# Optimization experiments

Measured on AMD Instinct MI355X. Metric: run time of the kernel, lower is better.

## Reference

```python
import jax, jax.numpy as jnp
import numpy as np
from jax import lax

B, C, H, W = 8, 64, 128, 128
KS = 3          # kernel size
K = KS * KS     # kernel field = 9
PAD = 1


def conv2d(x, w, b):
    # x: [B,Cin,H,W], w: [Cout,Cin,kh,kw], 'same' 3x3 conv
    y = lax.conv_general_dilated(x, w, window_strides=(1, 1),
                                 padding=((PAD, PAD), (PAD, PAD)),
                                 dimension_numbers=('NCHW', 'OIHW', 'NCHW'))
    return y + b[None, :, None, None]


def modulated_deform_conv(x, offset, mask, weight, bias):
    # x:[B,C,H,W], offset:[B,2K,H,W] (dy,dx per tap), mask:[B,K,H,W]
    Bs, Cin, Hin, Win = x.shape
    off = offset.reshape(Bs, K, 2, Hin, Win)
    ky, kx = jnp.meshgrid(jnp.arange(KS), jnp.arange(KS), indexing='ij')
    ky = ky.reshape(K).astype(x.dtype)   # kernel tap row offsets 0..2
    kx = kx.reshape(K).astype(x.dtype)
    # sampling positions p = p0 + p_k + offset (stride=1, pad=1)
    py = (jnp.arange(Hin, dtype=x.dtype)[None, None, :, None] - PAD
          + ky[None, :, None, None] + off[:, :, 0])            # [B,K,H,W]
    px = (jnp.arange(Win, dtype=x.dtype)[None, None, None, :] - PAD
          + kx[None, :, None, None] + off[:, :, 1])            # [B,K,H,W]

    y0 = jnp.floor(py); x0 = jnp.floor(px)
    ly = py - y0; lx = px - x0                                  # frac parts
    y0i = y0.astype(jnp.int32); x0i = x0.astype(jnp.int32)

    x_flat = x.reshape(Bs, Cin, Hin * Win)

    def gather(iy, ix):
        valid = ((iy >= 0) & (iy < Hin) & (ix >= 0) & (ix < Win))
        flat = (jnp.clip(iy, 0, Hin - 1) * Win + jnp.clip(ix, 0, Win - 1))
        g = jax.vmap(lambda xb, ib: xb[:, ib])(x_flat, flat.reshape(Bs, -1))
        g = g.reshape(Bs, Cin, K, Hin, Win)
        return g * valid[:, None].astype(x.dtype)

    w00 = ((1 - ly) * (1 - lx))[:, None]  # [B,1,K,H,W]
    w01 = ((1 - ly) * lx)[:, None]
    w10 = (ly * (1 - lx))[:, None]
    w11 = (ly * lx)[:, None]

    val = (w00 * gather(y0i, x0i) + w01 * gather(y0i, x0i + 1)
           + w10 * gather(y0i + 1, x0i) + w11 * gather(y0i + 1, x0i + 1))
    val = val * mask[:, None]                                   # modulation
    out = jnp.einsum('ock,bckhw->bohw', weight.reshape(weight.shape[0], Cin, K), val)
    return out + bias[None, :, None, None]


def setup_inputs() -> dict:
    key = jax.random.key(0)
    ks = jax.random.split(key, 7)
    s = 0.05
    return {
        'x': jax.random.normal(ks[0], (B, C, H, W), jnp.float32),
        'w_om': jax.random.normal(ks[1], (3 * K, C, KS, KS), jnp.float32) * s,
        'b_om': jax.random.normal(ks[2], (3 * K,), jnp.float32) * s,
        'w_dc': jax.random.normal(ks[3], (C, C, KS, KS), jnp.float32) * s,
        'b_dc': jax.random.normal(ks[4], (C,), jnp.float32) * s,
        'w_c': jax.random.normal(ks[5], (C, C, KS, KS), jnp.float32) * s,
        'b_c': jax.random.normal(ks[6], (C,), jnp.float32) * s,
    }


def reference(x, w_om, b_om, w_dc, b_dc, w_c, b_c):
    om = conv2d(x, w_om, b_om)                       # [B,3K,H,W]
    offset, mask_raw = om[:, :2 * K], om[:, 2 * K:]
    mask = 2.0 * jax.nn.sigmoid(mask_raw)
    out = modulated_deform_conv(x, offset, mask, w_dc, b_dc)
    act = jnp.where(out > 0, out, 0.2 * out)         # LeakyReLU(0.2)
    return conv2d(act, w_c, b_c) + x
```

## Files before the change

kernel.cpp:

```cpp
#include <hip/hip_runtime.h>
#include <math.h>

#define Bn 8
#define Cn 64
#define Hn 128
#define Wn 128
#define HWn (Hn * Wn)

#define WOM_OFF 0
#define WDC_OFF 18432
#define WC_OFF 55296

typedef __attribute__((ext_vector_type(8))) short short8;
typedef __attribute__((ext_vector_type(4))) float floatx4;

__device__ __forceinline__ float bf2f(short s) {
  return __uint_as_float(((unsigned)(unsigned short)s) << 16);
}
__device__ __forceinline__ short f2bf(float f) {
  unsigned u = __float_as_uint(f);
  u += 0x7fff + ((u >> 16) & 1);
  return (short)(u >> 16);
}

__global__ __launch_bounds__(256) void k_prep_w(
    const float* __restrict__ w_om, const float* __restrict__ w_dc,
    const float* __restrict__ w_c, short* __restrict__ wt) {
  int idx = blockIdx.x * 256 + threadIdx.x;
  if (idx >= 92160) return;
  float v;
  if (idx < WDC_OFF) {
    int e = idx;
    int elem = e & 7, lane = (e >> 3) & 63, mt = (e >> 9) & 1, t = e >> 10;
    int kk = t % 9, cc = t / 9;
    int row = mt * 16 + (lane & 15);
    int cin = cc * 32 + (lane >> 4) * 8 + elem;
    v = (row < 27) ? w_om[(row * 64 + cin) * 9 + kk] : 0.f;
  } else {
    int e = (idx < WC_OFF) ? idx - WDC_OFF : idx - WC_OFF;
    const float* src = (idx < WC_OFF) ? w_dc : w_c;
    int elem = e & 7, lane = (e >> 3) & 63, mt = (e >> 9) & 3, t = e >> 11;
    int kk = t % 9, cc = t / 9;
    int row = mt * 16 + (lane & 15);
    int cin = cc * 32 + (lane >> 4) * 8 + elem;
    v = src[(row * 64 + cin) * 9 + kk];
  }
  wt[idx] = f2bf(v);
}

__global__ __launch_bounds__(256) void k_prep_x(const float* __restrict__ x,
                                                short* __restrict__ xT) {
  __shared__ float tile[64][129];
  const int bid = blockIdx.x;
  const int b = bid & 7, h = bid >> 3;
  const int tid = threadIdx.x;
  const float* xb = x + (size_t)b * 64 * HWn + h * Wn;
  for (int i = tid; i < 8192; i += 256) {
    int c = i >> 7, w = i & 127;
    tile[c][w] = xb[c * HWn + w];
  }
  __syncthreads();
  short* dst = xT + ((size_t)(b * Hn + h) * Wn) * 64;
  for (int i = tid; i < 2048; i += 256) {
    int w = i >> 4, c4 = (i & 15) * 4;
    short4 o;
    o.x = f2bf(tile[c4 + 0][w]);
    o.y = f2bf(tile[c4 + 1][w]);
    o.z = f2bf(tile[c4 + 2][w]);
    o.w = f2bf(tile[c4 + 3][w]);
    *(short4*)(dst + (size_t)w * 64 + c4) = o;
  }
}

__global__ __launch_bounds__(512, 4) void k_omdef(
    const short* __restrict__ xT, const short* __restrict__ wt,
    const float* __restrict__ b_om, const float* __restrict__ b_dc,
    short* __restrict__ actT) {
  __shared__ __attribute__((aligned(16))) short lw[18432];
  __shared__ float som[27 * 132];
  __shared__ unsigned sbw[4 * 1152];
  unsigned* sb01 = sbw;
  unsigned* sb23 = sbw + 1152;
  unsigned* sw01 = sbw + 2304;
  unsigned* sw23 = sbw + 3456;

  const int bid = blockIdx.x;
  const int b = bid & 7;
  const int h = bid >> 3;
  const int tid = threadIdx.x;
  const int wave = tid >> 6, lane = tid & 63, quad = lane >> 4, lr = lane & 15;
  const short* xb = xT + (size_t)b * HWn * 64;
  const int pxl = wave * 16 + lr;

  floatx4 zf = {0.f, 0.f, 0.f, 0.f};
  const short8 zz = (short8){0, 0, 0, 0, 0, 0, 0, 0};

  {
    const short8* src = (const short8*)(wt + WOM_OFF);
    short8* dst = (short8*)lw;
    for (int i = tid; i < 2304; i += 512) dst[i] = src[i];
  }
  __syncthreads();

  floatx4 aco[2] = {zf, zf};
  short8 pb0, pb1;
  {
    int gy = h - 1, gx = pxl - 1;
    bool ok = ((unsigned)gy < (unsigned)Hn) && ((unsigned)gx < (unsigned)Wn);
    int gyc = min(max(gy, 0), Hn - 1), gxc = min(max(gx, 0), Wn - 1);
    const short* rec = xb + (size_t)(gyc * Wn + gxc) * 64 + quad * 8;
    pb0 = *(const short8*)(rec);
    pb1 = *(const short8*)(rec + 32);
    if (!ok) { pb0 = zz; pb1 = zz; }
  }
#pragma unroll
  for (int kk = 0; kk < 9; ++kk) {
    short8 nb0, nb1;
    if (kk < 8) {
      int ky = (kk + 1) / 3, kx = (kk + 1) - ky * 3;
      int gy = h + ky - 1, gx = pxl + kx - 1;
      bool ok = ((unsigned)gy < (unsigned)Hn) && ((unsigned)gx < (unsigned)Wn);
      int gyc = min(max(gy, 0), Hn - 1), gxc = min(max(gx, 0), Wn - 1);
      const short* rec = xb + (size_t)(gyc * Wn + gxc) * 64 + quad * 8;
      nb0 = *(const short8*)(rec);
      nb1 = *(const short8*)(rec + 32);
      if (!ok) { nb0 = zz; nb1 = zz; }
    }
    short8 a00 = *(const short8*)&lw[((0 * 9 + kk) * 2 + 0) * 512 + lane * 8];
    short8 a01v = *(const short8*)&lw[((0 * 9 + kk) * 2 + 1) * 512 + lane * 8];
    aco[0] = __builtin_amdgcn_mfma_f32_16x16x32_bf16(a00, pb0, aco[0], 0, 0, 0);
    aco[1] = __builtin_amdgcn_mfma_f32_16x16x32_bf16(a01v, pb0, aco[1], 0, 0, 0);
    short8 a10 = *(const short8*)&lw[((1 * 9 + kk) * 2 + 0) * 512 + lane * 8];
    short8 a11 = *(const short8*)&lw[((1 * 9 + kk) * 2 + 1) * 512 + lane * 8];
    aco[0] = __builtin_amdgcn_mfma_f32_16x16x32_bf16(a10, pb1, aco[0], 0, 0, 0);
    aco[1] = __builtin_amdgcn_mfma_f32_16x16x32_bf16(a11, pb1, aco[1], 0, 0, 0);
    if (kk < 8) { pb0 = nb0; pb1 = nb1; }
  }
#pragma unroll
  for (int mt = 0; mt < 2; ++mt) {
#pragma unroll
    for (int rr = 0; rr < 4; ++rr) {
      int co = mt * 16 + quad * 4 + rr;
      if (co < 27) {
        float v = aco[mt][rr] + b_om[co];
        if (co >= 18) v = 2.f / (1.f + expf(-v));
        som[co * 132 + pxl] = v;
      }
    }
  }
  __syncthreads();

  {
    const short8* src = (const short8*)(wt + WDC_OFF);
    short8* dst = (short8*)lw;
    for (int i = tid; i < 2304; i += 512) dst[i] = src[i];
  }
  for (int pr = tid; pr < 1152; pr += 512) {
    int k = pr >> 7, p = pr & 127;
    float offy = som[(2 * k) * 132 + p];
    float offx = som[(2 * k + 1) * 132 + p];
    float m = som[(18 + k) * 132 + p];
    float py = (float)(h - 1 + (k / 3)) + offy;
    float px_ = (float)(p - 1 + (k % 3)) + offx;
    float fy = floorf(py), fx = floorf(px_);
    float ly = py - fy, lx = px_ - fx;
    int iy0 = (int)fy, ix0 = (int)fx;
    int iy1 = iy0 + 1, ix1 = ix0 + 1;
    bool vy0 = (iy0 >= 0) && (iy0 < Hn);
    bool vy1 = (iy1 >= 0) && (iy1 < Hn);
    bool vx0 = (ix0 >= 0) && (ix0 < Wn);
    bool vx1 = (ix1 >= 0) && (ix1 < Wn);
    unsigned cy0 = (unsigned)min(max(iy0, 0), Hn - 1);
    unsigned cy1 = (unsigned)min(max(iy1, 0), Hn - 1);
    unsigned cx0 = (unsigned)min(max(ix0, 0), Wn - 1);
    unsigned cx1 = (unsigned)min(max(ix1, 0), Wn - 1);
    sb01[pr] = (cy0 * Wn + cx0) | ((cy0 * Wn + cx1) << 16);
    sb23[pr] = (cy1 * Wn + cx0) | ((cy1 * Wn + cx1) << 16);
    float u0 = (vy0 && vx0) ? (1.f - ly) * (1.f - lx) * m : 0.f;
    float u1 = (vy0 && vx1) ? (1.f - ly) * lx * m : 0.f;
    float u2 = (vy1 && vx0) ? ly * (1.f - lx) * m : 0.f;
    float u3 = (vy1 && vx1) ? ly * lx * m : 0.f;
    sw01[pr] = (unsigned)(unsigned short)f2bf(u0) |
               ((unsigned)(unsigned short)f2bf(u1) << 16);
    sw23[pr] = (unsigned)(unsigned short)f2bf(u2) |
               ((unsigned)(unsigned short)f2bf(u3) << 16);
  }
  __syncthreads();

  floatx4 acc[4] = {zf, zf, zf, zf};
  for (int cc = 0; cc < 2; ++cc) {
    const int co = cc * 32 + quad * 8;
    unsigned uw01 = sw01[pxl], uw23 = sw23[pxl];
    short8 q0, q1, q2, q3;
    {
      unsigned a01 = sb01[pxl], a23 = sb23[pxl];
      q0 = *(const short8*)(xb + (size_t)(a01 & 0xFFFF) * 64 + co);
      q1 = *(const short8*)(xb + (size_t)(a01 >> 16) * 64 + co);
      q2 = *(const short8*)(xb + (size_t)(a23 & 0xFFFF) * 64 + co);
      q3 = *(const short8*)(xb + (size_t)(a23 >> 16) * 64 + co);
    }
    if (cc) {
      __syncthreads();
      const short8* src = (const short8*)(wt + WDC_OFF + 18432);
      short8* dst = (short8*)lw;
      for (int i = tid; i < 2304; i += 512) dst[i] = src[i];
      __syncthreads();
    }
#pragma unroll 3
    for (int kk = 0; kk < 9; ++kk) {
      unsigned nw01, nw23;
      short8 n0, n1, n2, n3;
      if (kk < 8) {
        int pr = (kk + 1) * 128 + pxl;
        unsigned na01 = sb01[pr], na23 = sb23[pr];
        nw01 = sw01[pr];
        nw23 = sw23[pr];
        n0 = *(const short8*)(xb + (size_t)(na01 & 0xFFFF) * 64 + co);
        n1 = *(const short8*)(xb + (size_t)(na01 >> 16) * 64 + co);
        n2 = *(const short8*)(xb + (size_t)(na23 & 0xFFFF) * 64 + co);
        n3 = *(const short8*)(xb + (size_t)(na23 >> 16) * 64 + co);
      }
      float u0 = bf2f((short)(uw01 & 0xFFFF));
      float u1 = bf2f((short)(uw01 >> 16));
      float u2 = bf2f((short)(uw23 & 0xFFFF));
      float u3 = bf2f((short)(uw23 >> 16));
      short8 bf;
#pragma unroll
      for (int e = 0; e < 8; ++e) {
        float f = u0 * bf2f(q0[e]) + u1 * bf2f(q1[e]) + u2 * bf2f(q2[e]) +
                  u3 * bf2f(q3[e]);
        bf[e] = f2bf(f);
      }
#pragma unroll
      for (int mt = 0; mt < 4; ++mt) {
        short8 am = *(const short8*)&lw[(kk * 4 + mt) * 512 + lane * 8];
        acc[mt] = __builtin_amdgcn_mfma_f32_16x16x32_bf16(am, bf, acc[mt], 0, 0, 0);
      }
      if (kk < 8) {
        uw01 = nw01; uw23 = nw23;
        q0 = n0; q1 = n1; q2 = n2; q3 = n3;
      }
    }
  }

  short* ab = actT + ((size_t)(b * Hn + h) * Wn) * 64;
#pragma unroll
  for (int mt = 0; mt < 4; ++mt) {
    int c0 = mt * 16 + quad * 4;
    short4 o;
    float v;
    v = acc[mt][0] + b_dc[c0 + 0]; o.x = f2bf(v > 0.f ? v : 0.2f * v);
    v = acc[mt][1] + b_dc[c0 + 1]; o.y = f2bf(v > 0.f ? v : 0.2f * v);
    v = acc[mt][2] + b_dc[c0 + 2]; o.z = f2bf(v > 0.f ? v : 0.2f * v);
    v = acc[mt][3] + b_dc[c0 + 3]; o.w = f2bf(v > 0.f ? v : 0.2f * v);
    *(short4*)(ab + (size_t)pxl * 64 + c0) = o;
  }
}

__global__ __launch_bounds__(512, 4) void k_conv_out(
    const short* __restrict__ actT, const short* __restrict__ wt,
    const float* __restrict__ b_c, const float* __restrict__ x,
    float* __restrict__ out) {
  __shared__ __attribute__((aligned(16))) short lw[18432];

  const int bid = blockIdx.x;
  const int b = bid & 7;
  const int h = bid >> 3;
  const int tid = threadIdx.x;
  const int wave = tid >> 6, lane = tid & 63, quad = lane >> 4, lr = lane & 15;
  const short* ab = actT + (size_t)b * HWn * 64;
  const int pxl = wave * 16 + lr;

  floatx4 zf = {0.f, 0.f, 0.f, 0.f};
  const short8 zz = (short8){0, 0, 0, 0, 0, 0, 0, 0};
  floatx4 acc[4] = {zf, zf, zf, zf};

  for (int cc = 0; cc < 2; ++cc) {
    const int co = cc * 32 + quad * 8;
    short8 pbf;
    {
      int gy = h - 1, gx = pxl - 1;
      bool ok = ((unsigned)gy < (unsigned)Hn) && ((unsigned)gx < (unsigned)Wn);
      int gyc = min(max(gy, 0), Hn - 1), gxc = min(max(gx, 0), Wn - 1);
      pbf = *(const short8*)(ab + (size_t)(gyc * Wn + gxc) * 64 + co);
      if (!ok) pbf = zz;
    }
    if (cc) __syncthreads();
    {
      const short8* src = (const short8*)(wt + WC_OFF + cc * 18432);
      short8* dst = (short8*)lw;
      for (int i = tid; i < 2304; i += 512) dst[i] = src[i];
    }
    __syncthreads();
#pragma unroll
    for (int kk = 0; kk < 9; ++kk) {
      short8 nbf;
      if (kk < 8) {
        int ky = (kk + 1) / 3, kx = (kk + 1) - ky * 3;
        int gy = h + ky - 1, gx = pxl + kx - 1;
        bool ok = ((unsigned)gy < (unsigned)Hn) && ((unsigned)gx < (unsigned)Wn);
        int gyc = min(max(gy, 0), Hn - 1), gxc = min(max(gx, 0), Wn - 1);
        nbf = *(const short8*)(ab + (size_t)(gyc * Wn + gxc) * 64 + co);
        if (!ok) nbf = zz;
      }
#pragma unroll
      for (int mt = 0; mt < 4; ++mt) {
        short8 am = *(const short8*)&lw[(kk * 4 + mt) * 512 + lane * 8];
        acc[mt] = __builtin_amdgcn_mfma_f32_16x16x32_bf16(am, pbf, acc[mt], 0, 0, 0);
      }
      if (kk < 8) pbf = nbf;
    }
  }
  __syncthreads();

  float* ot = (float*)lw;
#pragma unroll
  for (int mt = 0; mt < 4; ++mt) {
#pragma unroll
    for (int rr = 0; rr < 4; ++rr) {
      ot[(mt * 16 + quad * 4 + rr) * 132 + pxl] = acc[mt][rr];
    }
  }
  __syncthreads();

  const int row = tid >> 3, seg = tid & 7;
  const float bias = b_c[row];
  const size_t gbase = ((size_t)(b * 64 + row) * Hn + h) * Wn + seg * 16;
  const float* xr = x + gbase;
  float* op = out + gbase;
#pragma unroll
  for (int j = 0; j < 4; ++j) {
    floatx4 t = *(const floatx4*)&ot[row * 132 + seg * 16 + j * 4];
    floatx4 xv = *(const floatx4*)&xr[j * 4];
    t = t + xv;
    t[0] += bias; t[1] += bias; t[2] += bias; t[3] += bias;
    *(floatx4*)&op[j * 4] = t;
  }
}

extern "C" void kernel_launch(void* const* d_in, const int* in_sizes, int n_in,
                              void* d_out, int out_size, void* d_ws,
                              size_t ws_size, hipStream_t stream) {
  const float* x = (const float*)d_in[0];
  const float* w_om = (const float*)d_in[1];
  const float* b_om = (const float*)d_in[2];
  const float* w_dc = (const float*)d_in[3];
  const float* b_dc = (const float*)d_in[4];
  const float* w_c = (const float*)d_in[5];
  const float* b_c = (const float*)d_in[6];
  float* out = (float*)d_out;

  short* xT = (short*)d_ws;
  short* actT = xT + (size_t)Bn * HWn * 64;
  short* wt = actT + (size_t)Bn * HWn * 64;

  k_prep_w<<<dim3(360), 256, 0, stream>>>(w_om, w_dc, w_c, wt);
  k_prep_x<<<dim3(1024), 256, 0, stream>>>(x, xT);
  k_omdef<<<dim3(1024), 512, 0, stream>>>(xT, wt, b_om, b_dc, actT);
  k_conv_out<<<dim3(1024), 512, 0, stream>>>(actT, wt, b_c, x, out);
}
```

Baseline: 217.3 us.

## Stage activation rows in swizzled LDS and read conv weights directly from global

```diff
diff --git a/kernel.cpp b/kernel.cpp
--- a/kernel.cpp
+++ b/kernel.cpp
@@ -261,7 +261,7 @@
     const short* __restrict__ actT, const short* __restrict__ wt,
     const float* __restrict__ b_c, const float* __restrict__ x,
     float* __restrict__ out) {
-  __shared__ __attribute__((aligned(16))) short lw[18432];
+  __shared__ __attribute__((aligned(16))) short rows[24576];
 
   const int bid = blockIdx.x;
   const int b = bid & 7;
@@ -274,46 +274,41 @@
   floatx4 zf = {0.f, 0.f, 0.f, 0.f};
   const short8 zz = (short8){0, 0, 0, 0, 0, 0, 0, 0};
   floatx4 acc[4] = {zf, zf, zf, zf};
-
+  short8* rows8 = (short8*)rows;
+
+  {
+    const short8* ar8 = (const short8*)ab;
+    for (int i = tid; i < 3072; i += 512) {
+      int rr = i >> 10, c = i & 1023;
+      int px = c >> 3, sl = c & 7;
+      int gy = min(max(h - 1 + rr, 0), Hn - 1);
+      short8 v = ar8[(size_t)(gy * Wn + px) * 8 + sl];
+      rows8[(rr << 10) + (px << 3) + (sl ^ (px & 7))] = v;
+    }
+  }
+  __syncthreads();
+
+#pragma unroll
   for (int cc = 0; cc < 2; ++cc) {
-    const int co = cc * 32 + quad * 8;
-    short8 pbf;
-    {
-      int gy = h - 1, gx = pxl - 1;
-      bool ok = ((unsigned)gy < (unsigned)Hn) && ((unsigned)gx < (unsigned)Wn);
-      int gyc = min(max(gy, 0), Hn - 1), gxc = min(max(gx, 0), Wn - 1);
-      pbf = *(const short8*)(ab + (size_t)(gyc * Wn + gxc) * 64 + co);
-      if (!ok) pbf = zz;
-    }
-    if (cc) __syncthreads();
-    {
-      const short8* src = (const short8*)(wt + WC_OFF + cc * 18432);
-      short8* dst = (short8*)lw;
-      for (int i = tid; i < 2304; i += 512) dst[i] = src[i];
-    }
-    __syncthreads();
 #pragma unroll
     for (int kk = 0; kk < 9; ++kk) {
-      short8 nbf;
-      if (kk < 8) {
-        int ky = (kk + 1) / 3, kx = (kk + 1) - ky * 3;
-        int gy = h + ky - 1, gx = pxl + kx - 1;
-        bool ok = ((unsigned)gy < (unsigned)Hn) && ((unsigned)gx < (unsigned)Wn);
-        int gyc = min(max(gy, 0), Hn - 1), gxc = min(max(gx, 0), Wn - 1);
-        nbf = *(const short8*)(ab + (size_t)(gyc * Wn + gxc) * 64 + co);
-        if (!ok) nbf = zz;
-      }
+      int ky = kk / 3, kx = kk - ky * 3;
+      int gy = h + ky - 1, gxx = pxl + kx - 1;
+      bool ok = ((unsigned)gy < (unsigned)Hn) && ((unsigned)gxx < (unsigned)Wn);
+      int gxc = min(max(gxx, 0), Wn - 1);
+      short8 bf = rows8[(ky << 10) + (gxc << 3) + ((cc * 4 + quad) ^ (gxc & 7))];
+      if (!ok) bf = zz;
 #pragma unroll
       for (int mt = 0; mt < 4; ++mt) {
-        short8 am = *(const short8*)&lw[(kk * 4 + mt) * 512 + lane * 8];
-        acc[mt] = __builtin_amdgcn_mfma_f32_16x16x32_bf16(am, pbf, acc[mt], 0, 0, 0);
-      }
-      if (kk < 8) pbf = nbf;
-    }
-  }
-  __syncthreads();
-
-  float* ot = (float*)lw;
+        short8 am = *(const short8*)(wt + WC_OFF + cc * 18432 +
+                                     (kk * 4 + mt) * 512 + lane * 8);
+        acc[mt] = __builtin_amdgcn_mfma_f32_16x16x32_bf16(am, bf, acc[mt], 0, 0, 0);
+      }
+    }
+  }
+  __syncthreads();
+
+  float* ot = (float*)rows;
 #pragma unroll
   for (int mt = 0; mt < 4; ++mt) {
 #pragma unroll
```

Result: no change. 219.0 us (+0.8%).
